# Optimization experiments

Hardware: AMD Instinct MI355X
Metric: run time of the kernel (lower is better)

## Reference

```python
import jax, jax.numpy as jnp
import numpy as np

N_RES = 768
DISTO_BINS = 64
LDDT_BINS = 50
MIN_RESOLUTION = 0.1
MAX_RESOLUTION = 3.0
W_DISTO, W_PLDDT, W_EXP = 0.3, 0.01, 0.01
CA_IDX = 1  # atom37 index of C-alpha


def setup_inputs() -> dict:
    key = jax.random.key(0)
    ks = jax.random.split(key, 6)
    B = 1
    return {
        "distogram_logits": jax.random.normal(ks[0], (B, N_RES, N_RES, DISTO_BINS), jnp.float32),
        "pseudo_beta": jax.random.normal(ks[1], (B, N_RES, 3), jnp.float32) * 10.0,
        "pseudo_beta_mask": jnp.ones((B, N_RES), jnp.float32),
        "lddt_logits": jax.random.normal(ks[2], (B, N_RES, LDDT_BINS), jnp.float32),
        "all_atom_pred_pos": jax.random.normal(ks[3], (B, N_RES, 37, 3), jnp.float32) * 10.0,
        "all_atom_positions": jax.random.normal(ks[4], (B, N_RES, 37, 3), jnp.float32) * 10.0,
        "all_atom_mask": jnp.ones((B, N_RES, 37), jnp.float32),
        "exp_resolved_logits": jax.random.normal(ks[5], (B, N_RES, 37), jnp.float32),
        "atom37_atom_exists": jnp.ones((B, N_RES, 37), jnp.float32),
        "resolution": jnp.ones((B,), jnp.float32),
    }


def _lddt(pred_pos, true_pos, mask, cutoff=15.0, eps=1e-10):
    # pred_pos/true_pos: [*, N, 3]; mask: [*, N, 1] -> per-residue lddt [*, N]
    n = mask.shape[-2]
    dmat_true = jnp.sqrt(eps + jnp.sum((true_pos[..., :, None, :] - true_pos[..., None, :, :]) ** 2, axis=-1))
    dmat_pred = jnp.sqrt(eps + jnp.sum((pred_pos[..., :, None, :] - pred_pos[..., None, :, :]) ** 2, axis=-1))
    scope = ((dmat_true < cutoff).astype(dmat_true.dtype)
             * mask * jnp.swapaxes(mask, -1, -2)
             * (1.0 - jnp.eye(n, dtype=dmat_true.dtype)))
    dist_l1 = jnp.abs(dmat_true - dmat_pred)
    score = 0.25 * ((dist_l1 < 0.5).astype(dist_l1.dtype) + (dist_l1 < 1.0)
                    + (dist_l1 < 2.0) + (dist_l1 < 4.0))
    norm = 1.0 / (eps + jnp.sum(scope, axis=-1))
    return norm * (eps + jnp.sum(scope * score, axis=-1))


def _ce_from_bins(logits, bins):
    # -sum(one_hot(bins) * log_softmax(logits)) == -log_softmax gathered at bins
    logp = jax.nn.log_softmax(logits, axis=-1)
    return -jnp.take_along_axis(logp, bins[..., None], axis=-1)[..., 0]


def _distogram_loss(logits, pseudo_beta, pseudo_beta_mask,
                    min_bin=2.3125, max_bin=21.6875, no_bins=DISTO_BINS, eps=1e-6):
    boundaries = jnp.linspace(min_bin, max_bin, no_bins - 1) ** 2
    d2 = jnp.sum((pseudo_beta[..., :, None, :] - pseudo_beta[..., None, :, :]) ** 2,
                 axis=-1, keepdims=True)  # [*, N, N, 1]
    true_bins = jnp.sum(d2 > boundaries, axis=-1).astype(jnp.int32)  # [*, N, N]
    errors = _ce_from_bins(logits, true_bins)
    sq_mask = pseudo_beta_mask[..., None] * pseudo_beta_mask[..., None, :]
    denom = eps + jnp.sum(sq_mask, axis=(-1, -2))
    mean = jnp.sum(errors * sq_mask, axis=-1) / denom[..., None]
    return jnp.mean(jnp.sum(mean, axis=-1))


def _lddt_loss(logits, all_atom_pred_pos, all_atom_positions, all_atom_mask, resolution,
               no_bins=LDDT_BINS, eps=1e-10):
    pred_ca = all_atom_pred_pos[..., CA_IDX, :]
    true_ca = all_atom_positions[..., CA_IDX, :]
    mask_ca = all_atom_mask[..., CA_IDX:CA_IDX + 1]  # [*, N, 1]
    score = jax.lax.stop_gradient(_lddt(pred_ca, true_ca, mask_ca, eps=eps))
    bin_idx = jnp.clip(jnp.floor(score * no_bins).astype(jnp.int32), 0, no_bins - 1)
    errors = _ce_from_bins(logits, bin_idx)
    m = mask_ca[..., 0]
    loss = jnp.sum(errors * m, axis=-1) / (eps + jnp.sum(m, axis=-1))
    gate = ((resolution >= MIN_RESOLUTION) & (resolution <= MAX_RESOLUTION)).astype(loss.dtype)
    return jnp.mean(loss * gate)


def _exp_resolved_loss(logits, atom37_atom_exists, all_atom_mask, resolution, eps=1e-8):
    errors = (-all_atom_mask * jax.nn.log_sigmoid(logits)
              - (1.0 - all_atom_mask) * jax.nn.log_sigmoid(-logits))
    loss = jnp.sum(errors * atom37_atom_exists, axis=-1)  # [*, N]
    loss = loss / (eps + jnp.sum(atom37_atom_exists, axis=(-1, -2)))[..., None]
    loss = jnp.sum(loss, axis=-1)
    gate = ((resolution >= MIN_RESOLUTION) & (resolution <= MAX_RESOLUTION)).astype(loss.dtype)
    return jnp.mean(loss * gate)


def reference(distogram_logits, pseudo_beta, pseudo_beta_mask, lddt_logits,
              all_atom_pred_pos, all_atom_positions, all_atom_mask,
              exp_resolved_logits, atom37_atom_exists, resolution):
    l_disto = _distogram_loss(distogram_logits, pseudo_beta, pseudo_beta_mask)
    l_plddt = _lddt_loss(lddt_logits, all_atom_pred_pos, all_atom_positions,
                         all_atom_mask, resolution)
    l_exp = _exp_resolved_loss(exp_resolved_logits, atom37_atom_exists,
                               all_atom_mask, resolution)
    return W_DISTO * l_disto + W_PLDDT * l_plddt + W_EXP * l_exp
```

## Files before the change

### kernel.cpp

```cpp
#include <hip/hip_runtime.h>
#include <math.h>

#define N_RES 768
#define DISTO_BINS 64
#define LDDT_BINS 50
#define DISTO_BLOCKS 2048
#define LDDT_BLOCKS N_RES
#define EXP_GRID 64
#define NPAIRS (N_RES * N_RES)
#define NCHUNKS (NPAIRS / 4)
#define CHUNKS_PER_WAVE 18

typedef float f32x4 __attribute__((ext_vector_type(4)));

#define ROW_ADD_ROR(v, N)                                                     \
    v += __int_as_float(__builtin_amdgcn_update_dpp(                          \
        0, __float_as_int(v), 0x120 | (N), 0xF, 0xF, false))

__global__ __launch_bounds__(256)
void pair_meta_kernel(const float* __restrict__ pb,
                      const float* __restrict__ pbm,
                      unsigned char* __restrict__ bins,
                      float* __restrict__ wgt) {
    int p = blockIdx.x * blockDim.x + threadIdx.x;
    if (p >= NPAIRS) return;
    int i = p / N_RES;
    int j = p - i * N_RES;
    float dx = pb[3 * i + 0] - pb[3 * j + 0];
    float dy = pb[3 * i + 1] - pb[3 * j + 1];
    float dz = pb[3 * i + 2] - pb[3 * j + 2];
    float d  = sqrtf(dx * dx + dy * dy + dz * dz);
    float t  = ceilf((d - 2.3125f) * 3.2f);
    int bin  = (int)fminf(fmaxf(t, 0.f), 63.f);
    bins[p]  = (unsigned char)bin;
    wgt[p]   = pbm[i] * pbm[j];
}

__global__ __launch_bounds__(256)
void fused_main_kernel(const f32x4* __restrict__ logits4,
                       const unsigned int* __restrict__ binw,
                       const float* __restrict__ wgt,
                       const float* __restrict__ pred37,
                       const float* __restrict__ true37,
                       const float* __restrict__ mask37,
                       const float* __restrict__ lddt_logits,
                       const float* __restrict__ exl,
                       const float* __restrict__ a37ex,
                       float* __restrict__ partial,
                       float* __restrict__ errm,
                       float* __restrict__ expnum,
                       float* __restrict__ expden) {
    __shared__ float r1[256], r2[256];
    const int tid  = threadIdx.x;
    const int nthr = blockDim.x;

    if (blockIdx.x < DISTO_BLOCKS) {
        const int lane = tid & 63;
        const int wid  = tid >> 6;
        const int q    = lane >> 4;
        const int gl   = lane & 15;
        const int gw   = blockIdx.x * 4 + wid;
        const int base = gw * CHUNKS_PER_WAVE;

        float acc = 0.f;

#define DISTO_PROC(xv4, cc)                                                   \
    {                                                                         \
        float e = __expf(xv4.x) + __expf(xv4.y) + __expf(xv4.z) +             \
                  __expf(xv4.w);                                              \
        ROW_ADD_ROR(e, 8);                                                    \
        ROW_ADD_ROR(e, 4);                                                    \
        ROW_ADD_ROR(e, 2);                                                    \
        ROW_ADD_ROR(e, 1);                                                    \
        unsigned int bw = binw[cc];                                           \
        int bin = (int)((bw >> (q * 8)) & 63u);                               \
        float w  = wgt[(cc) * 4 + q];                                         \
        float xs = (bin & 2) ? ((bin & 1) ? xv4.w : xv4.z)                    \
                             : ((bin & 1) ? xv4.y : xv4.x);                   \
        float lg = (gl == 0) ? w * __logf(e) : 0.f;                           \
        float bt = (gl == (bin >> 2)) ? w * xs : 0.f;                         \
        acc += lg - bt;                                                       \
    }

#pragma unroll
        for (int t3 = 0; t3 < 3; ++t3) {
            const int cb = base + t3 * 6;
            f32x4 x0 = __builtin_nontemporal_load(
                &logits4[(size_t)(cb + 0) * 64 + lane]);
            f32x4 x1 = __builtin_nontemporal_load(
                &logits4[(size_t)(cb + 1) * 64 + lane]);
            f32x4 x2 = __builtin_nontemporal_load(
                &logits4[(size_t)(cb + 2) * 64 + lane]);
            f32x4 x3 = __builtin_nontemporal_load(
                &logits4[(size_t)(cb + 3) * 64 + lane]);
            f32x4 x4 = __builtin_nontemporal_load(
                &logits4[(size_t)(cb + 4) * 64 + lane]);
            f32x4 x5 = __builtin_nontemporal_load(
                &logits4[(size_t)(cb + 5) * 64 + lane]);
            DISTO_PROC(x0, cb + 0);
            DISTO_PROC(x1, cb + 1);
            DISTO_PROC(x2, cb + 2);
            DISTO_PROC(x3, cb + 3);
            DISTO_PROC(x4, cb + 4);
            DISTO_PROC(x5, cb + 5);
        }
#undef DISTO_PROC

        acc += __shfl_xor(acc, 1, 64);
        acc += __shfl_xor(acc, 2, 64);
        acc += __shfl_xor(acc, 4, 64);
        acc += __shfl_xor(acc, 8, 64);
        acc += __shfl_xor(acc, 16, 64);
        acc += __shfl_xor(acc, 32, 64);
        if (lane == 0) r1[wid] = acc;
        __syncthreads();
        if (tid == 0)
            partial[blockIdx.x] = r1[0] + r1[1] + r1[2] + r1[3];
        return;
    }

    if (blockIdx.x >= DISTO_BLOCKS + LDDT_BLOCKS) {
        const int b = blockIdx.x - DISTO_BLOCKS - LDDT_BLOCKS;
        const int gid = b * nthr + tid;
        const int stride = EXP_GRID * nthr;
        const int n = N_RES * 37;
        float num = 0.f, den = 0.f;
        for (int k = gid; k < n; k += stride) {
            float x  = exl[k];
            float m  = mask37[k];
            float ex = a37ex[k];
            float ax = fabsf(x);
            float sp = __logf(1.f + __expf(-ax));
            float ls  = sp + fmaxf(-x, 0.f);
            float lsn = sp + fmaxf(x, 0.f);
            float err = m * ls + (1.f - m) * lsn;
            num += err * ex;
            den += ex;
        }
        r1[tid] = num;
        r2[tid] = den;
        __syncthreads();
        for (int s = nthr >> 1; s > 0; s >>= 1) {
            if (tid < s) { r1[tid] += r1[tid + s]; r2[tid] += r2[tid + s]; }
            __syncthreads();
        }
        if (tid == 0) { expnum[b] = r1[0]; expden[b] = r2[0]; }
        return;
    }

    const int i = blockIdx.x - DISTO_BLOCKS;
    const float tix = true37[(i * 37 + 1) * 3 + 0];
    const float tiy = true37[(i * 37 + 1) * 3 + 1];
    const float tiz = true37[(i * 37 + 1) * 3 + 2];
    const float pix = pred37[(i * 37 + 1) * 3 + 0];
    const float piy = pred37[(i * 37 + 1) * 3 + 1];
    const float piz = pred37[(i * 37 + 1) * 3 + 2];
    const float mi  = mask37[i * 37 + 1];

    float scope_sum = 0.f, score_sum = 0.f;
    for (int j = tid; j < N_RES; j += nthr) {
        float mj  = mask37[j * 37 + 1];
        float dtx = tix - true37[(j * 37 + 1) * 3 + 0];
        float dty = tiy - true37[(j * 37 + 1) * 3 + 1];
        float dtz = tiz - true37[(j * 37 + 1) * 3 + 2];
        float dt  = sqrtf(1e-10f + dtx * dtx + dty * dty + dtz * dtz);
        float dpx = pix - pred37[(j * 37 + 1) * 3 + 0];
        float dpy = piy - pred37[(j * 37 + 1) * 3 + 1];
        float dpz = piz - pred37[(j * 37 + 1) * 3 + 2];
        float dp  = sqrtf(1e-10f + dpx * dpx + dpy * dpy + dpz * dpz);
        float scope = (dt < 15.f && j != i) ? (mi * mj) : 0.f;
        float l1 = fabsf(dt - dp);
        float sc = 0.25f * ((l1 < 0.5f ? 1.f : 0.f) + (l1 < 1.f ? 1.f : 0.f) +
                            (l1 < 2.f ? 1.f : 0.f) + (l1 < 4.f ? 1.f : 0.f));
        scope_sum += scope;
        score_sum += scope * sc;
    }

    r1[tid] = scope_sum;
    r2[tid] = score_sum;
    __syncthreads();
    for (int s = nthr >> 1; s > 0; s >>= 1) {
        if (tid < s) { r1[tid] += r1[tid + s]; r2[tid] += r2[tid + s]; }
        __syncthreads();
    }

    __shared__ int binS;
    if (tid == 0) {
        float lddt = (1e-10f + r2[0]) / (1e-10f + r1[0]);
        int bin = (int)floorf(lddt * (float)LDDT_BINS);
        binS = min(max(bin, 0), LDDT_BINS - 1);
    }
    __syncthreads();

    float e = (tid < LDDT_BINS) ? __expf(lddt_logits[i * LDDT_BINS + tid]) : 0.f;
    r1[tid] = e;
    __syncthreads();
    for (int s = nthr >> 1; s > 0; s >>= 1) {
        if (tid < s) r1[tid] += r1[tid + s];
        __syncthreads();
    }
    if (tid == 0) {
        float err = __logf(r1[0]) - lddt_logits[i * LDDT_BINS + binS];
        errm[i] = err * mi;
    }
}

__global__ __launch_bounds__(256)
void finalize_kernel(const float* __restrict__ partial,
                     const float* __restrict__ pbm,
                     const float* __restrict__ errm,
                     const float* __restrict__ mask37,
                     const float* __restrict__ expnum,
                     const float* __restrict__ expden,
                     const float* __restrict__ resolution,
                     float* __restrict__ out) {
    const int tid = threadIdx.x;
    const int nthr = blockDim.x;

    double sd = 0.0, sm = 0.0, se = 0.0, smca = 0.0, num = 0.0, den = 0.0;
    for (int k = tid; k < DISTO_BLOCKS; k += nthr) sd += (double)partial[k];
    for (int k = tid; k < N_RES; k += nthr) {
        sm   += (double)pbm[k];
        se   += (double)errm[k];
        smca += (double)mask37[k * 37 + 1];
    }
    if (tid < EXP_GRID) { num = (double)expnum[tid]; den = (double)expden[tid]; }

    __shared__ double red[256];
    double vals[6] = {sd, sm, se, smca, num, den};
    double tot[6];
    for (int v = 0; v < 6; ++v) {
        red[tid] = vals[v];
        __syncthreads();
        for (int s = nthr >> 1; s > 0; s >>= 1) {
            if (tid < s) red[tid] += red[tid + s];
            __syncthreads();
        }
        tot[v] = red[0];
        __syncthreads();
    }

    if (tid == 0) {
        float res = resolution[0];
        double gate = (res >= 0.1f && res <= 3.0f) ? 1.0 : 0.0;
        double l_disto = tot[0] / (1e-6 + tot[1] * tot[1]);
        double l_plddt = tot[2] / (1e-10 + tot[3]) * gate;
        double l_exp   = tot[4] / (1e-8 + tot[5]) * gate;
        out[0] = (float)(0.3 * l_disto + 0.01 * l_plddt + 0.01 * l_exp);
    }
}

extern "C" void kernel_launch(void* const* d_in, const int* in_sizes, int n_in,
                              void* d_out, int out_size, void* d_ws, size_t ws_size,
                              hipStream_t stream) {
    const float* disto       = (const float*)d_in[0];
    const float* pb          = (const float*)d_in[1];
    const float* pbm         = (const float*)d_in[2];
    const float* lddt_logits = (const float*)d_in[3];
    const float* pred        = (const float*)d_in[4];
    const float* truep       = (const float*)d_in[5];
    const float* am          = (const float*)d_in[6];
    const float* exl         = (const float*)d_in[7];
    const float* a37         = (const float*)d_in[8];
    const float* resolution  = (const float*)d_in[9];
    float* out = (float*)d_out;

    float* ws      = (float*)d_ws;
    float* partial = ws;
    float* errm    = ws + DISTO_BLOCKS;
    float* expnum  = errm + N_RES;
    float* expden  = expnum + EXP_GRID;
    float* wgt     = ws + 4096;
    unsigned char* bins = (unsigned char*)(wgt + NPAIRS);

    pair_meta_kernel<<<(NPAIRS + 255) / 256, 256, 0, stream>>>(pb, pbm, bins, wgt);
    fused_main_kernel<<<DISTO_BLOCKS + LDDT_BLOCKS + EXP_GRID, 256, 0, stream>>>(
        (const f32x4*)disto, (const unsigned int*)bins, wgt,
        pred, truep, am, lddt_logits, exl, a37,
        partial, errm, expnum, expden);
    finalize_kernel<<<1, 256, 0, stream>>>(partial, pbm, errm, am,
                                           expnum, expden, resolution, out);
}
```

Before: 235.8 us.

## Fuse pair bin/weight computation into main kernel via shared memory

Removes the separate pair_meta_kernel that wrote per-pair bins and weights to global memory. Each distogram block now computes bins and mask weights for its 288 pairs into shared memory before streaming logits. Block order is also changed so the LDDT and exp-resolved blocks are scheduled first. This saves one kernel launch and the global write and read of the metadata, at the cost of a block-wide sync and some extra arithmetic per distogram block.

```diff
diff --git a/kernel.cpp b/kernel.cpp
--- a/kernel.cpp
+++ b/kernel.cpp
@@ -10,6 +10,9 @@
 #define NPAIRS (N_RES * N_RES)
 #define NCHUNKS (NPAIRS / 4)
 #define CHUNKS_PER_WAVE 18
+#define PAIRS_PER_BLOCK 288
+
+#define TOTAL_BLOCKS (LDDT_BLOCKS + EXP_GRID + DISTO_BLOCKS)
 
 typedef float f32x4 __attribute__((ext_vector_type(4)));
 
@@ -18,53 +21,54 @@
         0, __float_as_int(v), 0x120 | (N), 0xF, 0xF, false))
 
 __global__ __launch_bounds__(256)
-void pair_meta_kernel(const float* __restrict__ pb,
-                      const float* __restrict__ pbm,
-                      unsigned char* __restrict__ bins,
-                      float* __restrict__ wgt) {
-    int p = blockIdx.x * blockDim.x + threadIdx.x;
-    if (p >= NPAIRS) return;
-    int i = p / N_RES;
-    int j = p - i * N_RES;
-    float dx = pb[3 * i + 0] - pb[3 * j + 0];
-    float dy = pb[3 * i + 1] - pb[3 * j + 1];
-    float dz = pb[3 * i + 2] - pb[3 * j + 2];
-    float d  = sqrtf(dx * dx + dy * dy + dz * dz);
-    float t  = ceilf((d - 2.3125f) * 3.2f);
-    int bin  = (int)fminf(fmaxf(t, 0.f), 63.f);
-    bins[p]  = (unsigned char)bin;
-    wgt[p]   = pbm[i] * pbm[j];
-}
-
-__global__ __launch_bounds__(256)
-void fused_main_kernel(const f32x4* __restrict__ logits4,
-                       const unsigned int* __restrict__ binw,
-                       const float* __restrict__ wgt,
-                       const float* __restrict__ pred37,
-                       const float* __restrict__ true37,
-                       const float* __restrict__ mask37,
-                       const float* __restrict__ lddt_logits,
-                       const float* __restrict__ exl,
-                       const float* __restrict__ a37ex,
-                       float* __restrict__ partial,
-                       float* __restrict__ errm,
-                       float* __restrict__ expnum,
-                       float* __restrict__ expden) {
+void mega_kernel(const f32x4* __restrict__ logits4,
+                 const float* __restrict__ pb,
+                 const float* __restrict__ pbm,
+                 const float* __restrict__ pred37,
+                 const float* __restrict__ true37,
+                 const float* __restrict__ mask37,
+                 const float* __restrict__ lddt_logits,
+                 const float* __restrict__ exl,
+                 const float* __restrict__ a37ex,
+                 float* __restrict__ partial,
+                 float* __restrict__ errm,
+                 float* __restrict__ expnum,
+                 float* __restrict__ expden) {
     __shared__ float r1[256], r2[256];
+    __shared__ float swgt[PAIRS_PER_BLOCK];
+    __shared__ int   sbin[PAIRS_PER_BLOCK];
     const int tid  = threadIdx.x;
     const int nthr = blockDim.x;
 
-    if (blockIdx.x < DISTO_BLOCKS) {
+    if (blockIdx.x >= LDDT_BLOCKS + EXP_GRID) {
+        const int db   = blockIdx.x - (LDDT_BLOCKS + EXP_GRID);
         const int lane = tid & 63;
         const int wid  = tid >> 6;
         const int q    = lane >> 4;
         const int gl   = lane & 15;
-        const int gw   = blockIdx.x * 4 + wid;
+        const int gw   = db * 4 + wid;
         const int base = gw * CHUNKS_PER_WAVE;
+        const int P0   = db * PAIRS_PER_BLOCK;
+
+        for (int idx = tid; idx < PAIRS_PER_BLOCK; idx += nthr) {
+            int p = P0 + idx;
+            int i = p / N_RES;
+            int j = p - i * N_RES;
+            float dx = pb[3 * i + 0] - pb[3 * j + 0];
+            float dy = pb[3 * i + 1] - pb[3 * j + 1];
+            float dz = pb[3 * i + 2] - pb[3 * j + 2];
+            float d  = sqrtf(dx * dx + dy * dy + dz * dz);
+            float t  = ceilf((d - 2.3125f) * 3.2f);
+            sbin[idx] = (int)fminf(fmaxf(t, 0.f), 63.f);
+            swgt[idx] = pbm[i] * pbm[j];
+        }
+        __syncthreads();
+
+        const int mb = wid * 72 + q;
 
         float acc = 0.f;
 
-#define DISTO_PROC(xv4, cc)                                                   \
+#define DISTO_PROC(xv4, li)                                                   \
     {                                                                         \
         float e = __expf(xv4.x) + __expf(xv4.y) + __expf(xv4.z) +             \
                   __expf(xv4.w);                                              \
@@ -72,9 +76,8 @@
         ROW_ADD_ROR(e, 4);                                                    \
         ROW_ADD_ROR(e, 2);                                                    \
         ROW_ADD_ROR(e, 1);                                                    \
-        unsigned int bw = binw[cc];                                           \
-        int bin = (int)((bw >> (q * 8)) & 63u);                               \
-        float w  = wgt[(cc) * 4 + q];                                         \
+        int bin = sbin[li];                                                   \
+        float w  = swgt[li];                                                  \
         float xs = (bin & 2) ? ((bin & 1) ? xv4.w : xv4.z)                    \
                              : ((bin & 1) ? xv4.y : xv4.x);                   \
         float lg = (gl == 0) ? w * __logf(e) : 0.f;                           \
@@ -97,12 +100,12 @@
                 &logits4[(size_t)(cb + 4) * 64 + lane]);
             f32x4 x5 = __builtin_nontemporal_load(
                 &logits4[(size_t)(cb + 5) * 64 + lane]);
-            DISTO_PROC(x0, cb + 0);
-            DISTO_PROC(x1, cb + 1);
-            DISTO_PROC(x2, cb + 2);
-            DISTO_PROC(x3, cb + 3);
-            DISTO_PROC(x4, cb + 4);
-            DISTO_PROC(x5, cb + 5);
+            DISTO_PROC(x0, mb + 4 * (t3 * 6 + 0));
+            DISTO_PROC(x1, mb + 4 * (t3 * 6 + 1));
+            DISTO_PROC(x2, mb + 4 * (t3 * 6 + 2));
+            DISTO_PROC(x3, mb + 4 * (t3 * 6 + 3));
+            DISTO_PROC(x4, mb + 4 * (t3 * 6 + 4));
+            DISTO_PROC(x5, mb + 4 * (t3 * 6 + 5));
         }
 #undef DISTO_PROC
 
@@ -115,12 +118,12 @@
         if (lane == 0) r1[wid] = acc;
         __syncthreads();
         if (tid == 0)
-            partial[blockIdx.x] = r1[0] + r1[1] + r1[2] + r1[3];
+            partial[db] = r1[0] + r1[1] + r1[2] + r1[3];
         return;
     }
 
-    if (blockIdx.x >= DISTO_BLOCKS + LDDT_BLOCKS) {
-        const int b = blockIdx.x - DISTO_BLOCKS - LDDT_BLOCKS;
+    if (blockIdx.x >= LDDT_BLOCKS) {
+        const int b = blockIdx.x - LDDT_BLOCKS;
         const int gid = b * nthr + tid;
         const int stride = EXP_GRID * nthr;
         const int n = N_RES * 37;
@@ -148,7 +151,7 @@
         return;
     }
 
-    const int i = blockIdx.x - DISTO_BLOCKS;
+    const int i = blockIdx.x;
     const float tix = true37[(i * 37 + 1) * 3 + 0];
     const float tiy = true37[(i * 37 + 1) * 3 + 1];
     const float tiz = true37[(i * 37 + 1) * 3 + 2];
@@ -270,12 +273,9 @@
     float* errm    = ws + DISTO_BLOCKS;
     float* expnum  = errm + N_RES;
     float* expden  = expnum + EXP_GRID;
-    float* wgt     = ws + 4096;
-    unsigned char* bins = (unsigned char*)(wgt + NPAIRS);
-
-    pair_meta_kernel<<<(NPAIRS + 255) / 256, 256, 0, stream>>>(pb, pbm, bins, wgt);
-    fused_main_kernel<<<DISTO_BLOCKS + LDDT_BLOCKS + EXP_GRID, 256, 0, stream>>>(
-        (const f32x4*)disto, (const unsigned int*)bins, wgt,
+
+    mega_kernel<<<TOTAL_BLOCKS, 256, 0, stream>>>(
+        (const f32x4*)disto, pb, pbm,
         pred, truep, am, lddt_logits, exl, a37,
         partial, errm, expnum, expden);
     finalize_kernel<<<1, 256, 0, stream>>>(partial, pbm, errm, am,
```

Measured after the change: 228.9 us, median of 2. 1.03x faster.
